# Kernel optimization log

Hardware: AMD Instinct MI355X
Metric: run time of the kernel (lower is better)

Reference implementation:

```python
import jax, jax.numpy as jnp
import numpy as np

N_HEADS = 16
HEAD_DIM = 64
THRESHOLD = 0.5
TAU = 12.5
N_FHN_STEPS = 2


def fhn_imex_step(v, w, I, a, b, dt, tau):
    # IMEX step of FitzHugh-Nagumo dynamics:
    #   explicit update for v (nonlinear), implicit for w (linear in w)
    #   dv/dt = v - v^3/3 - w + I
    #   dw/dt = (v + a - b*w) / tau
    v_new = v + dt * (v - v ** 3 / 3.0 - w + I)
    w_new = (w + (dt / tau) * (v_new + a)) / (1.0 + (dt / tau) * b)
    return v_new, w_new


def setup_inputs() -> dict:
    key = jax.random.key(0)
    k1, k2, k3 = jax.random.split(key, 3)
    B, T, D = 2, 2048, 1024
    x = jax.random.normal(k1, (B, T, D), dtype=jnp.float32)
    Wqkv = jax.random.normal(k2, (3 * D, D), dtype=jnp.float32) * 0.02
    Wout = jax.random.normal(k3, (D, D), dtype=jnp.float32) * 0.02
    a = jnp.float32(0.7)
    b = jnp.float32(0.8)
    dt = jnp.float32(1.0)
    return {"x": x, "Wqkv": Wqkv, "Wout": Wout, "a": a, "b": b, "dt": dt}


def reference(x, Wqkv, Wout, a, b, dt):
    B, T, D = x.shape
    H, hd = N_HEADS, HEAD_DIM
    qkv = x @ Wqkv.T                              # (B, T, 3D)
    qkv = qkv.reshape(B, T, 3, H, hd)             # 'b t (three h d)'
    q = qkv[:, :, 0].transpose(0, 2, 1, 3)        # (B, H, T, hd)
    k = qkv[:, :, 1].transpose(0, 2, 1, 3)
    v = qkv[:, :, 2].transpose(0, 2, 1, 3)

    scores = jnp.einsum('bhtd,bhsd->bhts', q, k) / np.sqrt(hd).astype(np.float32)
    causal = jnp.triu(jnp.ones((T, T), dtype=bool), k=1)
    scores = jnp.where(causal[None, None], -jnp.inf, scores)
    attn_probs = jax.nn.softmax(scores, axis=-1)  # (B, H, T, T); dropout=0 -> identity

    attn_energy = attn_probs.sum(axis=-1)                              # (B, H, T)
    stim_scale = jnp.maximum(jnp.abs(attn_energy).max(axis=-1, keepdims=True), 1e-6)
    stimulus_normed = attn_energy / stim_scale
    threshold_gate = jax.nn.sigmoid((jnp.abs(attn_energy) - THRESHOLD) * 10.0)
    I = stimulus_normed * (0.1 + 0.9 * threshold_gate)                 # (B, H, T)
    I = jnp.broadcast_to(I[..., None], (B, H, T, hd))                  # expand to head_dim

    v_state = jnp.zeros_like(I)
    w_state = jnp.zeros_like(I)
    for _ in range(N_FHN_STEPS):
        v_state, w_state = fhn_imex_step(v_state, w_state, I, a, b, dt, TAU)

    fhn_gate = jax.nn.sigmoid(v_state.mean(axis=-1))[..., None]        # (B, H, T, 1)
    attn_probs = attn_probs * (0.5 + 0.5 * fhn_gate)
    attn_probs = attn_probs / (attn_probs.sum(axis=-1, keepdims=True) + 1e-8)

    out = jnp.einsum('bhts,bhsd->bhtd', attn_probs, v)                 # (B, H, T, hd)
    out = out.transpose(0, 2, 1, 3).reshape(B, T, D)
    out = out @ Wout.T
    return out
```

## Files before the change

### kernel.cpp

```cpp
#include <hip/hip_runtime.h>

typedef unsigned short u16;
typedef __attribute__((ext_vector_type(8))) short bf16x8;
typedef __attribute__((ext_vector_type(4))) float f32x4;
typedef __attribute__((ext_vector_type(4))) unsigned short u16x4;
typedef __attribute__((ext_vector_type(4))) unsigned int u32x4;

__device__ __forceinline__ u16 f2bf(float f) {
    unsigned int u = __builtin_bit_cast(unsigned int, f);
    u += 0x7fffu + ((u >> 16) & 1u);
    return (u16)(u >> 16);
}

__device__ __forceinline__ float bf2f(u16 b) {
    unsigned int u = ((unsigned int)b) << 16;
    return __builtin_bit_cast(float, u);
}

__device__ __forceinline__ unsigned int cvt_pk_bf16(float lo, float hi) {
    unsigned int r;
    asm("v_cvt_pk_bf16_f32 %0, %1, %2" : "=v"(r) : "v"(lo), "v"(hi));
    return r;
}

__device__ __forceinline__ void gload_lds16(const u16* g, const u16* l) {
    __builtin_amdgcn_global_load_lds((const __attribute__((address_space(1))) void*)g,
                                     (__attribute__((address_space(3))) void*)l,
                                     16, 0, 0);
}

__global__ __launch_bounds__(256) void cvt_f32_bf16(const float* __restrict__ in,
                                                    u16* __restrict__ out, int n4) {
    int i = blockIdx.x * blockDim.x + threadIdx.x;
    int stride = gridDim.x * blockDim.x;
    for (; i < n4; i += stride) {
        float4 v = reinterpret_cast<const float4*>(in)[i];
        u16x4 o = { f2bf(v.x), f2bf(v.y), f2bf(v.z), f2bf(v.w) };
        reinterpret_cast<u16x4*>(out)[i] = o;
    }
}

template <typename OutT>
__global__ __launch_bounds__(256) void gemm_bt(const u16* __restrict__ A, const u16* __restrict__ B,
                                               OutT* __restrict__ C, int M, int N, int K) {
    __shared__ u16 ldsA[128 * 64];
    __shared__ u16 ldsB[128 * 64];
    const int tid = threadIdx.x;
    const int lane = tid & 63;
    const int wid = tid >> 6;
    const int wm = wid >> 1, wn = wid & 1;
    const int lq = lane & 15, lg = lane >> 4;

    const int nbn = N >> 7;
    const int id = blockIdx.x;
    const int idp = (id & 7) * ((int)gridDim.x >> 3) + (id >> 3);
    const int bm = (idp / nbn) * 128;
    const int bn = (idp % nbn) * 128;

    const u16* aSrc[4];
    const u16* bSrc[4];
    int dstOff[4];
#pragma unroll
    for (int j = 0; j < 4; ++j) {
        int item = j * 256 + tid;
        int row = item >> 3;
        int c16 = item & 7;
        aSrc[j] = A + (size_t)(bm + row) * K + c16 * 8;
        bSrc[j] = B + (size_t)(bn + row) * K + c16 * 8;
        dstOff[j] = (j * 256 + (tid & ~63)) * 16;
    }

    f32x4 acc[4][4] = {};
    for (int k0 = 0; k0 < K; k0 += 64) {
        if (k0) __syncthreads();
#pragma unroll
        for (int j = 0; j < 4; ++j) {
            gload_lds16(aSrc[j], (const u16*)((const char*)ldsA + dstOff[j]));
            gload_lds16(bSrc[j], (const u16*)((const char*)ldsB + dstOff[j]));
            aSrc[j] += 64;
            bSrc[j] += 64;
        }
        __syncthreads();
#pragma unroll
        for (int kk = 0; kk < 2; ++kk) {
            bf16x8 af[4], bfr[4];
#pragma unroll
            for (int m = 0; m < 4; ++m) {
                int row = wm * 64 + m * 16 + lq;
                af[m] = *(const bf16x8*)((const char*)ldsA + row * 128 + kk * 64 + lg * 16);
            }
#pragma unroll
            for (int n = 0; n < 4; ++n) {
                int row = wn * 64 + n * 16 + lq;
                bfr[n] = *(const bf16x8*)((const char*)ldsB + row * 128 + kk * 64 + lg * 16);
            }
#pragma unroll
            for (int m = 0; m < 4; ++m)
#pragma unroll
                for (int n = 0; n < 4; ++n)
                    acc[m][n] = __builtin_amdgcn_mfma_f32_16x16x32_bf16(af[m], bfr[n], acc[m][n], 0, 0, 0);
        }
    }

#pragma unroll
    for (int m = 0; m < 4; ++m) {
#pragma unroll
        for (int n = 0; n < 4; ++n) {
#pragma unroll
            for (int r = 0; r < 4; ++r) {
                int row = bm + wm * 64 + m * 16 + lg * 4 + r;
                int col = bn + wn * 64 + n * 16 + lq;
                float v = acc[m][n][r];
                if constexpr (sizeof(OutT) == 2)
                    C[(size_t)row * N + col] = (OutT)f2bf(v);
                else
                    C[(size_t)row * N + col] = (OutT)v;
            }
        }
    }
}

__global__ __launch_bounds__(256) void transpose_v(const u16* __restrict__ qkv, u16* __restrict__ vt) {
    __shared__ u16 tile[64][72];
    const int tb = blockIdx.x * 64;
    const int bh = blockIdx.y;
    const int b = bh >> 4, h = bh & 15;
    const u16* src = qkv + ((size_t)(b * 2048 + tb)) * 3072 + 2048 + h * 64;
    const int tid = threadIdx.x;
#pragma unroll
    for (int p = 0; p < 2; ++p) {
        int item = p * 256 + tid;
        int t = item >> 3, c = item & 7;
        bf16x8 v = *(const bf16x8*)(src + (size_t)t * 3072 + c * 8);
        *(bf16x8*)(&tile[t][c * 8]) = v;
    }
    __syncthreads();
    u16* dst = vt + ((size_t)bh * 64) * 2048 + tb;
#pragma unroll
    for (int p = 0; p < 2; ++p) {
        int item = p * 256 + tid;
        int d = item >> 3, tc = item & 7;
        bf16x8 o;
#pragma unroll
        for (int j = 0; j < 8; ++j) o[j] = (short)tile[tc * 8 + j][d];
        *(bf16x8*)(dst + (size_t)d * 2048 + tc * 8) = o;
    }
}

__global__ __launch_bounds__(256, 5) void fhn_attn(const u16* __restrict__ qkv, const u16* __restrict__ vt,
                                                   u16* __restrict__ attno,
                                                   u16* __restrict__ pO, float* __restrict__ pML) {
    __shared__ u16 kvbuf[2][2][64 * 64];
    const int id = blockIdx.x;
    const int xcd = id & 7;
    const int u = id >> 3;
    const int bh = xcd * 4 + (u & 3);
    const int unit = u >> 2;
    int qt, jb0, jb1, sidx;
    bool split;
    if (unit < 32) {
        qt = 31 - (unit >> 1);
        sidx = unit & 1;
        split = true;
        int n = qt + 1, hh = (n + 1) >> 1;
        jb0 = sidx ? hh : 0;
        jb1 = sidx ? n : hh;
    } else {
        qt = 47 - unit;
        sidx = 0;
        split = false;
        jb0 = 0;
        jb1 = qt + 1;
    }
    const int b = bh >> 4, h = bh & 15;
    const int tid = threadIdx.x;
    const int w = tid >> 6;
    const int lane = tid & 63;
    const int lq = lane & 15, lg = lane >> 4;
    const int qlo = qt * 64 + w * 16;
    const int tq = qlo + lq;

    bf16x8 qf[2];
    {
        const u16* qrow = qkv + ((size_t)(b * 2048 + tq)) * 3072 + h * 64;
        qf[0] = *(const bf16x8*)(qrow + lg * 8);
        qf[1] = *(const bf16x8*)(qrow + 32 + lg * 8);
#pragma unroll
        for (int kk = 0; kk < 2; ++kk)
#pragma unroll
            for (int j = 0; j < 8; ++j)
                qf[kk][j] = (short)f2bf(bf2f((u16)qf[kk][j]) * 0.1803368801f);
    }

    const int it0 = tid, it1 = 256 + tid;
    const int r0 = it0 >> 3, g0 = (it0 & 7) ^ (r0 & 7);
    const int r1 = it1 >> 3, g1 = (it1 & 7) ^ (r1 & 7);
    const int pr0 = (((r0 >> 4) & 1) << 5) | ((r0 & 12) << 1) | (((r0 >> 5) & 1) << 2) | (r0 & 3);
    const int pr1 = (((r1 >> 4) & 1) << 5) | ((r1 & 12) << 1) | (((r1 >> 5) & 1) << 2) | (r1 & 3);
    const u16* kS0 = qkv + ((size_t)(b * 2048 + jb0 * 64 + pr0)) * 3072 + 1024 + h * 64 + g0 * 8;
    const u16* kS1 = qkv + ((size_t)(b * 2048 + jb0 * 64 + pr1)) * 3072 + 1024 + h * 64 + g1 * 8;
    const u16* vS0 = vt + ((size_t)bh * 64 + r0) * 2048 + jb0 * 64 + g0 * 8;
    const u16* vS1 = vt + ((size_t)bh * 64 + r1) * 2048 + jb0 * 64 + g1 * 8;
    const int d0 = (it0 & ~63) * 8;
    const int d1 = (it1 & ~63) * 8;

#define STAGE(buf)                                            \
    do {                                                      \
        gload_lds16(kS0, &kvbuf[buf][0][d0]);                 \
        gload_lds16(kS1, &kvbuf[buf][0][d1]);                 \
        gload_lds16(vS0, &kvbuf[buf][1][d0]);                 \
        gload_lds16(vS1, &kvbuf[buf][1][d1]);                 \
        kS0 += 64 * 3072; kS1 += 64 * 3072;                   \
        vS0 += 64; vS1 += 64;                                 \
    } while (0)

    float m_run = -1e30f, l_run = 0.f;
    f32x4 oacc[4] = {};
    int cur = 0;

    STAGE(0);

    for (int jb = jb0; jb < jb1; ++jb) {
        asm volatile("s_waitcnt vmcnt(0)" ::: "memory");
        __builtin_amdgcn_s_barrier();
        __builtin_amdgcn_sched_barrier(0);
        if (jb + 1 < jb1) STAGE(cur ^ 1);

        const u16* kb = kvbuf[cur][0];
        const u16* vb = kvbuf[cur][1];

        float p[4][4];
        __builtin_amdgcn_s_setprio(1);
#pragma unroll
        for (int st = 0; st < 4; ++st) {
            int row = st * 16 + lq;
            f32x4 sacc = {};
            sacc = __builtin_amdgcn_mfma_f32_16x16x32_bf16(
                *(const bf16x8*)(kb + row * 64 + ((lg ^ (row & 7)) * 8)), qf[0], sacc, 0, 0, 0);
            sacc = __builtin_amdgcn_mfma_f32_16x16x32_bf16(
                *(const bf16x8*)(kb + row * 64 + (((4 + lg) ^ (row & 7)) * 8)), qf[1], sacc, 0, 0, 0);
#pragma unroll
            for (int r = 0; r < 4; ++r) p[st][r] = sacc[r];
        }
        __builtin_amdgcn_s_setprio(0);

        bf16x8 vf[2][4];
#pragma unroll
        for (int c = 0; c < 2; ++c)
#pragma unroll
            for (int nd = 0; nd < 4; ++nd) {
                int row = nd * 16 + lq;
                vf[c][nd] = *(const bf16x8*)(vb + row * 64 + (((c * 4 + lg) ^ (row & 7)) * 8));
            }

        if (jb == qt) {
#pragma unroll
            for (int st = 0; st < 4; ++st)
#pragma unroll
                for (int r = 0; r < 4; ++r) {
                    int s = jb * 64 + ((st & 1) << 5) + (lg << 3) + ((st >> 1) << 2) + r;
                    if (s > tq) p[st][r] = -1e30f;
                }
        }

        float mst[4];
#pragma unroll
        for (int st = 0; st < 4; ++st)
            mst[st] = fmaxf(fmaxf(p[st][0], p[st][1]), fmaxf(p[st][2], p[st][3]));
        float mloc = fmaxf(fmaxf(mst[0], mst[1]), fmaxf(mst[2], mst[3]));
        mloc = fmaxf(mloc, __shfl_xor(mloc, 16));
        mloc = fmaxf(mloc, __shfl_xor(mloc, 32));

        if (!__all(mloc - m_run <= 8.0f)) {
            float mnew = fmaxf(m_run, mloc);
            float scp = exp2f(m_run - mnew);
            m_run = mnew;
            l_run *= scp;
            float f0 = __shfl(scp, lg * 4 + 0);
            float f1 = __shfl(scp, lg * 4 + 1);
            float f2_ = __shfl(scp, lg * 4 + 2);
            float f3 = __shfl(scp, lg * 4 + 3);
#pragma unroll
            for (int nd = 0; nd < 4; ++nd) {
                oacc[nd][0] *= f0; oacc[nd][1] *= f1;
                oacc[nd][2] *= f2_; oacc[nd][3] *= f3;
            }
        }

        float lst[4];
#pragma unroll
        for (int st = 0; st < 4; ++st) {
#pragma unroll
            for (int r = 0; r < 4; ++r)
                p[st][r] = exp2f(p[st][r] - m_run);
            lst[st] = (p[st][0] + p[st][1]) + (p[st][2] + p[st][3]);
        }
        float lloc = (lst[0] + lst[1]) + (lst[2] + lst[3]);
        lloc += __shfl_xor(lloc, 16);
        lloc += __shfl_xor(lloc, 32);
        l_run += lloc;

        __builtin_amdgcn_s_setprio(1);
#pragma unroll
        for (int c = 0; c < 2; ++c) {
            u32x4 pw = { cvt_pk_bf16(p[c][0], p[c][1]),
                         cvt_pk_bf16(p[c][2], p[c][3]),
                         cvt_pk_bf16(p[c + 2][0], p[c + 2][1]),
                         cvt_pk_bf16(p[c + 2][2], p[c + 2][3]) };
            bf16x8 pa = __builtin_bit_cast(bf16x8, pw);
#pragma unroll
            for (int nd = 0; nd < 4; ++nd)
                oacc[nd] = __builtin_amdgcn_mfma_f32_16x16x32_bf16(pa, vf[c][nd], oacc[nd], 0, 0, 0);
        }
        __builtin_amdgcn_s_setprio(0);

        cur ^= 1;
    }
#undef STAGE

    if (split) {
        const int pidx = ((((bh << 4) | (qt - 16)) << 1) + sidx);
        u16* obase = pO + (size_t)pidx * 4096;
#pragma unroll
        for (int nd = 0; nd < 4; ++nd)
#pragma unroll
            for (int r = 0; r < 4; ++r) {
                int rt = w * 16 + lg * 4 + r;
                obase[rt * 64 + nd * 16 + lq] = f2bf(oacc[nd][r]);
            }
        if (lg == 0) {
            pML[pidx * 128 + w * 16 + lq] = m_run;
            pML[pidx * 128 + 64 + w * 16 + lq] = l_run;
        }
    } else {
        float li0 = 1.f / __shfl(l_run, lg * 4 + 0);
        float li1 = 1.f / __shfl(l_run, lg * 4 + 1);
        float li2 = 1.f / __shfl(l_run, lg * 4 + 2);
        float li3 = 1.f / __shfl(l_run, lg * 4 + 3);
#pragma unroll
        for (int nd = 0; nd < 4; ++nd) {
#pragma unroll
            for (int r = 0; r < 4; ++r) {
                int trow = qlo + lg * 4 + r;
                float li = (r == 0) ? li0 : (r == 1) ? li1 : (r == 2) ? li2 : li3;
                attno[((size_t)(b * 2048 + trow)) * 1024 + h * 64 + nd * 16 + lq] =
                    f2bf(oacc[nd][r] * li);
            }
        }
    }
}

__global__ __launch_bounds__(256) void attn_merge(const u16* __restrict__ pO, const float* __restrict__ pML,
                                                  u16* __restrict__ attno) {
    const int tilei = blockIdx.x;
    const int bh = tilei >> 4, q16 = tilei & 15;
    const int qt = 16 + q16;
    const int b = bh >> 4, h = bh & 15;
    const int p0 = tilei * 2, p1 = p0 + 1;
    const int t = threadIdx.x;
    const int rt = t >> 2;
    const int c0 = (t & 3) * 16;

    float m0 = pML[p0 * 128 + rt], l0 = pML[p0 * 128 + 64 + rt];
    float m1 = pML[p1 * 128 + rt], l1 = pML[p1 * 128 + 64 + rt];
    float M = fmaxf(m0, m1);
    float a0 = exp2f(m0 - M), a1 = exp2f(m1 - M);
    float inv = 1.f / (l0 * a0 + l1 * a1);
    a0 *= inv; a1 *= inv;

    const u16* O0 = pO + (size_t)p0 * 4096 + rt * 64 + c0;
    const u16* O1 = pO + (size_t)p1 * 4096 + rt * 64 + c0;
    u16* dst = attno + ((size_t)(b * 2048 + qt * 64 + rt)) * 1024 + h * 64 + c0;
#pragma unroll
    for (int half = 0; half < 2; ++half) {
        bf16x8 v0 = *(const bf16x8*)(O0 + half * 8);
        bf16x8 v1 = *(const bf16x8*)(O1 + half * 8);
        bf16x8 o;
#pragma unroll
        for (int j = 0; j < 8; ++j)
            o[j] = (short)f2bf(bf2f((u16)v0[j]) * a0 + bf2f((u16)v1[j]) * a1);
        *(bf16x8*)(dst + half * 8) = o;
    }
}

extern "C" void kernel_launch(void* const* d_in, const int* in_sizes, int n_in,
                              void* d_out, int out_size, void* d_ws, size_t ws_size,
                              hipStream_t stream) {
    const float* x    = (const float*)d_in[0];
    const float* Wqkv = (const float*)d_in[1];
    const float* Wout = (const float*)d_in[2];
    float* out = (float*)d_out;

    char* ws = (char*)d_ws;
    u16* xb    = (u16*)(ws + 0);
    u16* wqkvb = (u16*)(ws + 8388608);
    u16* woutb = (u16*)(ws + 14680064);
    u16* qkvb  = (u16*)(ws + 16777216);
    u16* vtb   = (u16*)(ws + 41943040);
    u16* attno = (u16*)(ws + 50331648);
    u16* pO    = xb;
    float* pML = (float*)wqkvb;

    cvt_f32_bf16<<<2048, 256, 0, stream>>>(x, xb, 4194304 / 4);
    cvt_f32_bf16<<<2048, 256, 0, stream>>>(Wqkv, wqkvb, 3145728 / 4);
    cvt_f32_bf16<<<1024, 256, 0, stream>>>(Wout, woutb, 1048576 / 4);

    gemm_bt<u16><<<768, 256, 0, stream>>>(xb, wqkvb, qkvb, 4096, 3072, 1024);

    transpose_v<<<dim3(32, 32), 256, 0, stream>>>(qkvb, vtb);

    fhn_attn<<<1536, 256, 0, stream>>>(qkvb, vtb, attno, pO, pML);

    attn_merge<<<512, 256, 0, stream>>>(pO, pML, attno);

    gemm_bt<float><<<256, 256, 0, stream>>>(attno, woutb, out, 4096, 1024, 1024);
}
```

Before: 135.9 us.

## Fuse conversion kernels, retile output GEMM, defer row-sum reduction in attention

Merges the three fp32-to-bf16 conversion launches into one kernel and templates the GEMM on tile sizes, so the output projection runs with 64x128 tiles across 512 blocks instead of 256. In the attention kernel, per-lane partial row sums are kept in a vector and cross-lane shuffled only once after the loop, which removes two shuffles per KV block. The occupancy hint for the attention kernel drops from 5 to 4 waves. The aim is less launch overhead and better CU fill for the small GEMM, at the cost of extra registers and possibly lower occupancy in attention.

```diff
diff --git a/kernel.cpp b/kernel.cpp
--- a/kernel.cpp
+++ b/kernel.cpp
@@ -29,87 +29,108 @@
                                      16, 0, 0);
 }
 
-__global__ __launch_bounds__(256) void cvt_f32_bf16(const float* __restrict__ in,
-                                                    u16* __restrict__ out, int n4) {
-    int i = blockIdx.x * blockDim.x + threadIdx.x;
-    int stride = gridDim.x * blockDim.x;
-    for (; i < n4; i += stride) {
-        float4 v = reinterpret_cast<const float4*>(in)[i];
+__global__ __launch_bounds__(256) void cvt3_f32_bf16(const float* __restrict__ a, u16* __restrict__ ab, int na4,
+                                                     const float* __restrict__ b, u16* __restrict__ bb, int nb4,
+                                                     const float* __restrict__ c, u16* __restrict__ cb, int nc4) {
+    const int stride = gridDim.x * blockDim.x;
+    int i0 = blockIdx.x * blockDim.x + threadIdx.x;
+    for (int i = i0; i < na4; i += stride) {
+        float4 v = reinterpret_cast<const float4*>(a)[i];
         u16x4 o = { f2bf(v.x), f2bf(v.y), f2bf(v.z), f2bf(v.w) };
-        reinterpret_cast<u16x4*>(out)[i] = o;
-    }
-}
-
-template <typename OutT>
+        reinterpret_cast<u16x4*>(ab)[i] = o;
+    }
+    for (int i = i0; i < nb4; i += stride) {
+        float4 v = reinterpret_cast<const float4*>(b)[i];
+        u16x4 o = { f2bf(v.x), f2bf(v.y), f2bf(v.z), f2bf(v.w) };
+        reinterpret_cast<u16x4*>(bb)[i] = o;
+    }
+    for (int i = i0; i < nc4; i += stride) {
+        float4 v = reinterpret_cast<const float4*>(c)[i];
+        u16x4 o = { f2bf(v.x), f2bf(v.y), f2bf(v.z), f2bf(v.w) };
+        reinterpret_cast<u16x4*>(cb)[i] = o;
+    }
+}
+
+template <int BM, int BN, typename OutT>
 __global__ __launch_bounds__(256) void gemm_bt(const u16* __restrict__ A, const u16* __restrict__ B,
                                                OutT* __restrict__ C, int M, int N, int K) {
-    __shared__ u16 ldsA[128 * 64];
-    __shared__ u16 ldsB[128 * 64];
+    __shared__ u16 ldsA[BM * 64];
+    __shared__ u16 ldsB[BN * 64];
+    constexpr int RA = BM * 8 / 256;
+    constexpr int RB = BN * 8 / 256;
+    constexpr int MF = BM / 32;
+    constexpr int NF = BN / 32;
     const int tid = threadIdx.x;
     const int lane = tid & 63;
     const int wid = tid >> 6;
     const int wm = wid >> 1, wn = wid & 1;
     const int lq = lane & 15, lg = lane >> 4;
 
-    const int nbn = N >> 7;
+    const int nbn = N / BN;
     const int id = blockIdx.x;
     const int idp = (id & 7) * ((int)gridDim.x >> 3) + (id >> 3);
-    const int bm = (idp / nbn) * 128;
-    const int bn = (idp % nbn) * 128;
-
-    const u16* aSrc[4];
-    const u16* bSrc[4];
-    int dstOff[4];
-#pragma unroll
-    for (int j = 0; j < 4; ++j) {
+    const int bm = (idp / nbn) * BM;
+    const int bn = (idp % nbn) * BN;
+
+    const u16* aSrc[RA];
+    const u16* bSrc[RB];
+    int dstOffA[RA], dstOffB[RB];
+#pragma unroll
+    for (int j = 0; j < RA; ++j) {
         int item = j * 256 + tid;
-        int row = item >> 3;
-        int c16 = item & 7;
-        aSrc[j] = A + (size_t)(bm + row) * K + c16 * 8;
-        bSrc[j] = B + (size_t)(bn + row) * K + c16 * 8;
-        dstOff[j] = (j * 256 + (tid & ~63)) * 16;
-    }
-
-    f32x4 acc[4][4] = {};
+        aSrc[j] = A + (size_t)(bm + (item >> 3)) * K + (item & 7) * 8;
+        dstOffA[j] = (j * 256 + (tid & ~63)) * 16;
+    }
+#pragma unroll
+    for (int j = 0; j < RB; ++j) {
+        int item = j * 256 + tid;
+        bSrc[j] = B + (size_t)(bn + (item >> 3)) * K + (item & 7) * 8;
+        dstOffB[j] = (j * 256 + (tid & ~63)) * 16;
+    }
+
+    f32x4 acc[MF][NF] = {};
     for (int k0 = 0; k0 < K; k0 += 64) {
         if (k0) __syncthreads();
 #pragma unroll
-        for (int j = 0; j < 4; ++j) {
-            gload_lds16(aSrc[j], (const u16*)((const char*)ldsA + dstOff[j]));
-            gload_lds16(bSrc[j], (const u16*)((const char*)ldsB + dstOff[j]));
+        for (int j = 0; j < RA; ++j) {
+            gload_lds16(aSrc[j], (const u16*)((const char*)ldsA + dstOffA[j]));
             aSrc[j] += 64;
+        }
+#pragma unroll
+        for (int j = 0; j < RB; ++j) {
+            gload_lds16(bSrc[j], (const u16*)((const char*)ldsB + dstOffB[j]));
             bSrc[j] += 64;
         }
         __syncthreads();
 #pragma unroll
         for (int kk = 0; kk < 2; ++kk) {
-            bf16x8 af[4], bfr[4];
-#pragma unroll
-            for (int m = 0; m < 4; ++m) {
-                int row = wm * 64 + m * 16 + lq;
+            bf16x8 af[MF], bfr[NF];
+#pragma unroll
+            for (int m = 0; m < MF; ++m) {
+                int row = wm * (BM / 2) + m * 16 + lq;
                 af[m] = *(const bf16x8*)((const char*)ldsA + row * 128 + kk * 64 + lg * 16);
             }
 #pragma unroll
-            for (int n = 0; n < 4; ++n) {
-                int row = wn * 64 + n * 16 + lq;
+            for (int n = 0; n < NF; ++n) {
+                int row = wn * (BN / 2) + n * 16 + lq;
                 bfr[n] = *(const bf16x8*)((const char*)ldsB + row * 128 + kk * 64 + lg * 16);
             }
 #pragma unroll
-            for (int m = 0; m < 4; ++m)
-#pragma unroll
-                for (int n = 0; n < 4; ++n)
+            for (int m = 0; m < MF; ++m)
+#pragma unroll
+                for (int n = 0; n < NF; ++n)
                     acc[m][n] = __builtin_amdgcn_mfma_f32_16x16x32_bf16(af[m], bfr[n], acc[m][n], 0, 0, 0);
         }
     }
 
 #pragma unroll
-    for (int m = 0; m < 4; ++m) {
-#pragma unroll
-        for (int n = 0; n < 4; ++n) {
+    for (int m = 0; m < MF; ++m) {
+#pragma unroll
+        for (int n = 0; n < NF; ++n) {
 #pragma unroll
             for (int r = 0; r < 4; ++r) {
-                int row = bm + wm * 64 + m * 16 + lg * 4 + r;
-                int col = bn + wn * 64 + n * 16 + lq;
+                int row = bm + wm * (BM / 2) + m * 16 + lg * 4 + r;
+                int col = bn + wn * (BN / 2) + n * 16 + lq;
                 float v = acc[m][n][r];
                 if constexpr (sizeof(OutT) == 2)
                     C[(size_t)row * N + col] = (OutT)f2bf(v);
@@ -147,7 +168,7 @@
     }
 }
 
-__global__ __launch_bounds__(256, 5) void fhn_attn(const u16* __restrict__ qkv, const u16* __restrict__ vt,
+__global__ __launch_bounds__(256, 4) void fhn_attn(const u16* __restrict__ qkv, const u16* __restrict__ vt,
                                                    u16* __restrict__ attno,
                                                    u16* __restrict__ pO, float* __restrict__ pML) {
     __shared__ u16 kvbuf[2][2][64 * 64];
@@ -214,7 +235,8 @@
         vS0 += 64; vS1 += 64;                                 \
     } while (0)
 
-    float m_run = -1e30f, l_run = 0.f;
+    float m_run = -1e30f;
+    f32x4 lacc = { 0.f, 0.f, 0.f, 0.f };
     f32x4 oacc[4] = {};
     int cur = 0;
 
@@ -275,7 +297,8 @@
             float mnew = fmaxf(m_run, mloc);
             float scp = exp2f(m_run - mnew);
             m_run = mnew;
-            l_run *= scp;
+#pragma unroll
+            for (int st = 0; st < 4; ++st) lacc[st] *= scp;
             float f0 = __shfl(scp, lg * 4 + 0);
             float f1 = __shfl(scp, lg * 4 + 1);
             float f2_ = __shfl(scp, lg * 4 + 2);
@@ -287,18 +310,13 @@
             }
         }
 
-        float lst[4];
 #pragma unroll
         for (int st = 0; st < 4; ++st) {
 #pragma unroll
             for (int r = 0; r < 4; ++r)
                 p[st][r] = exp2f(p[st][r] - m_run);
-            lst[st] = (p[st][0] + p[st][1]) + (p[st][2] + p[st][3]);
-        }
-        float lloc = (lst[0] + lst[1]) + (lst[2] + lst[3]);
-        lloc += __shfl_xor(lloc, 16);
-        lloc += __shfl_xor(lloc, 32);
-        l_run += lloc;
+            lacc[st] += (p[st][0] + p[st][1]) + (p[st][2] + p[st][3]);
+        }
 
         __builtin_amdgcn_s_setprio(1);
 #pragma unroll
@@ -317,6 +335,10 @@
         cur ^= 1;
     }
 #undef STAGE
+
+    float l_run = (lacc[0] + lacc[1]) + (lacc[2] + lacc[3]);
+    l_run += __shfl_xor(l_run, 16);
+    l_run += __shfl_xor(l_run, 32);
 
     if (split) {
         const int pidx = ((((bh << 4) | (qt - 16)) << 1) + sidx);
@@ -401,11 +423,11 @@
     u16* pO    = xb;
     float* pML = (float*)wqkvb;
 
-    cvt_f32_bf16<<<2048, 256, 0, stream>>>(x, xb, 4194304 / 4);
-    cvt_f32_bf16<<<2048, 256, 0, stream>>>(Wqkv, wqkvb, 3145728 / 4);
-    cvt_f32_bf16<<<1024, 256, 0, stream>>>(Wout, woutb, 1048576 / 4);
-
-    gemm_bt<u16><<<768, 256, 0, stream>>>(xb, wqkvb, qkvb, 4096, 3072, 1024);
+    cvt3_f32_bf16<<<2048, 256, 0, stream>>>(x, xb, 4194304 / 4,
+                                            Wqkv, wqkvb, 3145728 / 4,
+                                            Wout, woutb, 1048576 / 4);
+
+    gemm_bt<128, 128, u16><<<768, 256, 0, stream>>>(xb, wqkvb, qkvb, 4096, 3072, 1024);
 
     transpose_v<<<dim3(32, 32), 256, 0, stream>>>(qkvb, vtb);
 
@@ -413,5 +435,5 @@
 
     attn_merge<<<512, 256, 0, stream>>>(pO, pML, attno);
 
-    gemm_bt<float><<<256, 256, 0, stream>>>(attno, woutb, out, 4096, 1024, 1024);
-}
+    gemm_bt<64, 128, float><<<512, 256, 0, stream>>>(attno, woutb, out, 4096, 1024, 1024);
+}
```

After: 111.8 us (median of 2 runs). -17.7%, faster.
